# Performance work log

Measured on AMD Instinct MI355X. Metric: run time of the kernel, lower is better.

## Reference

```python
import jax, jax.numpy as jnp
import numpy as np

BLOCK_SIZE = 32
EPS = 1e-6


def setup_inputs() -> dict:
    key = jax.random.key(0)
    k1, k2, k3, k4, k5 = jax.random.split(key, 5)
    B, H, L, D = 2, 16, 4096, 128
    return {
        "query_states": jax.random.normal(k1, (B, H, L, D), dtype=jnp.float32),
        "key_states": jax.random.normal(k2, (B, H, L, D), dtype=jnp.float32),
        "value_states": jax.random.normal(k3, (B, H, L, D), dtype=jnp.float32),
        # learned params; init near torch defaults (ones/zeros) with small noise
        "phi_scale": 1.0 + 0.1 * jax.random.normal(k4, (H, 1, D), dtype=jnp.float32),
        "phi_bias": 0.1 * jax.random.normal(k5, (H, 1, D), dtype=jnp.float32),
    }


def _forward(query_states, key_states, value_states, phi_scale, phi_bias):
    B, H, L, D = query_states.shape
    bs = BLOCK_SIZE
    N = L // bs  # L chosen divisible by block_size (no padding path)

    def feature_map(x):  # x: (B,H,N,bs,D)
        # phi_scale (H,1,D) -> (H,1,1,D) broadcasts over (B,H,N,bs,D)
        y = jax.nn.elu(x * phi_scale[:, None] + phi_bias[:, None]) + 1.0
        return jnp.clip(y, 0.0, 10.0)

    q = query_states.reshape(B, H, N, bs, D)
    k = key_states.reshape(B, H, N, bs, D)
    v = value_states.reshape(B, H, N, bs, D)

    phi_q = feature_map(q)
    phi_k = feature_map(k)

    # move block axis to front for scan: (N,B,H,bs,D)
    pq = jnp.moveaxis(phi_q, 2, 0)
    pk = jnp.moveaxis(phi_k, 2, 0)
    vb = jnp.moveaxis(v, 2, 0)

    S0 = jnp.zeros((B, H, D, D), dtype=jnp.float32)
    Z0 = jnp.zeros((B, H, D), dtype=jnp.float32)

    def step(carry, inp):
        S, Z = carry
        pq_n, pk_n, v_n = inp  # each (B,H,bs,D)
        # block-causal, bidirectional within block: update state BEFORE output
        S = S + jnp.einsum('bhkd,bhke->bhde', pk_n, v_n)
        Z = Z + pk_n.sum(axis=-2)
        num = jnp.einsum('bhqd,bhde->bhqe', pq_n, S)
        den = jnp.maximum(jnp.einsum('bhqd,bhd->bhq', pq_n, Z), EPS)
        return (S, Z), num / den[..., None]

    _, out_blocks = jax.lax.scan(step, (S0, Z0), (pq, pk, vb))  # (N,B,H,bs,D)
    out = jnp.moveaxis(out_blocks, 0, 2).reshape(B, H, L, D)
    return out


def reference(query_states, key_states, value_states, phi_scale, phi_bias):
    return _forward(query_states, key_states, value_states, phi_scale, phi_bias)
```

## Files before the change

kernel.cpp:

```cpp
#include <hip/hip_runtime.h>
#include <stdint.h>

#define BH 32
#define LSEQ 4096
#define DDIM 128
#define BS 32
#define NBLK 128
#define CHUNKS 16
#define BLK_PER_CHUNK 8
#define STATE_SZ (DDIM*DDIM + DDIM)

typedef __attribute__((ext_vector_type(8))) short bf16x8;
typedef __attribute__((ext_vector_type(4))) float f32x4;

__device__ inline uint16_t f2bf(float f) {
    uint32_t x = __builtin_bit_cast(uint32_t, f);
    x += 0x7fffu + ((x >> 16) & 1u);
    return (uint16_t)(x >> 16);
}
__device__ inline float bflo(uint32_t w){ return __builtin_bit_cast(float, w << 16); }
__device__ inline float bfhi(uint32_t w){ return __builtin_bit_cast(float, w & 0xffff0000u); }

__device__ inline float phi_f(float x, float s, float b) {
    float y = fmaf(x, s, b);
    float pos = fminf(y + 1.0f, 10.0f);
    float neg = __expf(y);
    return (y > 0.0f) ? pos : neg;
}

#define SMEM_BYTES 62080

template<bool PHASE2>
__global__ __launch_bounds__(512, 4) void la_phase(
    const float* __restrict__ Q, const float* __restrict__ K,
    const float* __restrict__ V, const float* __restrict__ scale,
    const float* __restrict__ bias, float* __restrict__ states,
    float* __restrict__ out)
{
    extern __shared__ char smem[];
    uint16_t* S_bfT  = (uint16_t*)smem;
    uint16_t* pk_bf  = (uint16_t*)smem;
    uint16_t* v_bf   = (uint16_t*)(smem + 8704);
    uint16_t* pkT    = (uint16_t*)(smem + 34816);
    uint16_t* pq_bf  = pkT;
    uint16_t* vT     = (uint16_t*)(smem + 45056);
    float* Zl        = (float*)(smem + 55296);
    float* Zpart     = Zl + 128;
    float* den_part  = Zpart + 8*128;
    float* inv_den   = den_part + 32*16;

    const int tid  = threadIdx.x;
    const int bid  = blockIdx.x;
    const int bh   = bid >> 4;
    const int ch   = bid & 15;
    const int lane = tid & 63;
    const int wv   = tid >> 6;
    const int i15  = lane & 15;
    const int q4   = lane >> 4;

    const size_t base = (size_t)bh * LSEQ * DDIM;
    const int h = bh & 15;

    const int sr = tid >> 4;
    const int sc = (tid & 15) * 8;

    float sreg[8], breg[8];
    #pragma unroll
    for (int j = 0; j < 8; ++j) {
        sreg[j] = scale[h*DDIM + sc + j];
        breg[j] = bias[h*DDIM + sc + j];
    }

    f32x4 accS[8];
    float* stbase = states + (size_t)(bh*CHUNKS + ch) * STATE_SZ;

    if (PHASE2) {
        #pragma unroll
        for (int mt = 0; mt < 8; ++mt) {
            #pragma unroll
            for (int r = 0; r < 4; ++r) {
                int d = 16*mt + 4*q4 + r;
                accS[mt][r] = stbase[d*DDIM + 16*wv + i15];
            }
        }
        if (tid < 128) Zl[tid] = stbase[DDIM*DDIM + tid];
    } else {
        #pragma unroll
        for (int mt = 0; mt < 8; ++mt) accS[mt] = (f32x4){0.f,0.f,0.f,0.f};
        if (tid < 128) Zl[tid] = 0.f;
    }
    __syncthreads();

    for (int s = 0; s < BLK_PER_CHUNK; ++s) {
        const int blk = ch * BLK_PER_CHUNK + s;
        const size_t rowoff = base + (size_t)(blk*BS + sr) * DDIM + sc;

        {
            const float4 k0 = *(const float4*)(K + rowoff);
            const float4 k1 = *(const float4*)(K + rowoff + 4);
            const float4 v0 = *(const float4*)(V + rowoff);
            const float4 v1 = *(const float4*)(V + rowoff + 4);
            float kp[8] = {k0.x,k0.y,k0.z,k0.w,k1.x,k1.y,k1.z,k1.w};
            float vp[8] = {v0.x,v0.y,v0.z,v0.w,v1.x,v1.y,v1.z,v1.w};
            uint32_t pk[4], pv[4];
            #pragma unroll
            for (int j = 0; j < 4; ++j) {
                uint32_t lo = f2bf(phi_f(kp[2*j],   sreg[2*j],   breg[2*j]));
                uint32_t hi = f2bf(phi_f(kp[2*j+1], sreg[2*j+1], breg[2*j+1]));
                pk[j] = lo | (hi << 16);
                lo = f2bf(vp[2*j]); hi = f2bf(vp[2*j+1]);
                pv[j] = lo | (hi << 16);
            }
            *(uint4*)&pk_bf[sr*136 + sc] = *(uint4*)pk;
            *(uint4*)&v_bf [sr*136 + sc] = *(uint4*)pv;
        }
        __syncthreads();

        {
            const int dp  = tid & 63;
            const int seg = tid >> 6;
            const int r0  = seg * 4;
            uint32_t w0 = *(const uint32_t*)&pk_bf[(r0+0)*136 + 2*dp];
            uint32_t w1 = *(const uint32_t*)&pk_bf[(r0+1)*136 + 2*dp];
            uint32_t w2 = *(const uint32_t*)&pk_bf[(r0+2)*136 + 2*dp];
            uint32_t w3 = *(const uint32_t*)&pk_bf[(r0+3)*136 + 2*dp];
            uint2 lo, hi;
            lo.x = (w0 & 0xffffu) | (w1 << 16);
            lo.y = (w2 & 0xffffu) | (w3 << 16);
            hi.x = (w0 >> 16) | (w1 & 0xffff0000u);
            hi.y = (w2 >> 16) | (w3 & 0xffff0000u);
            *(uint2*)&pkT[(2*dp+0)*40 + r0] = lo;
            *(uint2*)&pkT[(2*dp+1)*40 + r0] = hi;
            Zpart[seg*128 + 2*dp+0] = bflo(w0)+bflo(w1)+bflo(w2)+bflo(w3);
            Zpart[seg*128 + 2*dp+1] = bfhi(w0)+bfhi(w1)+bfhi(w2)+bfhi(w3);
            w0 = *(const uint32_t*)&v_bf[(r0+0)*136 + 2*dp];
            w1 = *(const uint32_t*)&v_bf[(r0+1)*136 + 2*dp];
            w2 = *(const uint32_t*)&v_bf[(r0+2)*136 + 2*dp];
            w3 = *(const uint32_t*)&v_bf[(r0+3)*136 + 2*dp];
            lo.x = (w0 & 0xffffu) | (w1 << 16);
            lo.y = (w2 & 0xffffu) | (w3 << 16);
            hi.x = (w0 >> 16) | (w1 & 0xffff0000u);
            hi.y = (w2 >> 16) | (w3 & 0xffff0000u);
            *(uint2*)&vT[(2*dp+0)*40 + r0] = lo;
            *(uint2*)&vT[(2*dp+1)*40 + r0] = hi;
        }
        __syncthreads();

        if (tid < 128) {
            float z = Zl[tid];
            #pragma unroll
            for (int g = 0; g < 8; ++g) z += Zpart[g*128 + tid];
            Zl[tid] = z;
        }
        {
            bf16x8 bv = *(const bf16x8*)&vT[(16*wv + i15)*40 + 8*q4];
            #pragma unroll
            for (int mt = 0; mt < 8; ++mt) {
                bf16x8 av = *(const bf16x8*)&pkT[(16*mt + i15)*40 + 8*q4];
                accS[mt] = __builtin_amdgcn_mfma_f32_16x16x32_bf16(av, bv, accS[mt], 0, 0, 0);
            }
        }

        if (PHASE2) {
            __syncthreads();

            {
                const float4 a0 = *(const float4*)(Q + rowoff);
                const float4 a1 = *(const float4*)(Q + rowoff + 4);
                float qp[8] = {a0.x,a0.y,a0.z,a0.w,a1.x,a1.y,a1.z,a1.w};
                uint32_t pq[4];
                #pragma unroll
                for (int j = 0; j < 4; ++j) {
                    uint32_t lo = f2bf(phi_f(qp[2*j],   sreg[2*j],   breg[2*j]));
                    uint32_t hi = f2bf(phi_f(qp[2*j+1], sreg[2*j+1], breg[2*j+1]));
                    pq[j] = lo | (hi << 16);
                }
                *(uint4*)&pq_bf[sr*136 + sc] = *(uint4*)pq;
            }
            #pragma unroll
            for (int mt = 0; mt < 8; ++mt) {
                uint2 o;
                o.x = (uint32_t)f2bf(accS[mt][0]) | ((uint32_t)f2bf(accS[mt][1]) << 16);
                o.y = (uint32_t)f2bf(accS[mt][2]) | ((uint32_t)f2bf(accS[mt][3]) << 16);
                *(uint2*)&S_bfT[(16*wv + i15)*136 + 16*mt + 4*q4] = o;
            }
            __syncthreads();

            f32x4 acc2[2];
            acc2[0] = (f32x4){0.f,0.f,0.f,0.f};
            acc2[1] = (f32x4){0.f,0.f,0.f,0.f};
            #pragma unroll
            for (int ks = 0; ks < 4; ++ks) {
                bf16x8 sb = *(const bf16x8*)&S_bfT[(16*wv + i15)*136 + 32*ks + 8*q4];
                #pragma unroll
                for (int qt = 0; qt < 2; ++qt) {
                    bf16x8 qa = *(const bf16x8*)&pq_bf[(16*qt + i15)*136 + 32*ks + 8*q4];
                    acc2[qt] = __builtin_amdgcn_mfma_f32_16x16x32_bf16(qa, sb, acc2[qt], 0, 0, 0);
                }
            }
            {
                const int dq = tid >> 4;
                const int pt = tid & 15;
                float sden = 0.f;
                #pragma unroll
                for (int j = 0; j < 4; ++j) {
                    uint32_t w = *(const uint32_t*)&pq_bf[dq*136 + 8*pt + 2*j];
                    sden += bflo(w) * Zl[8*pt + 2*j] + bfhi(w) * Zl[8*pt + 2*j + 1];
                }
                den_part[dq*16 + pt] = sden;
            }
            __syncthreads();
            if (tid < 32) {
                float sden = 0.f;
                #pragma unroll
                for (int j = 0; j < 16; ++j) sden += den_part[tid*16 + j];
                inv_den[tid] = 1.0f / fmaxf(sden, 1e-6f);
            }
            __syncthreads();

            #pragma unroll
            for (int qt = 0; qt < 2; ++qt) {
                #pragma unroll
                for (int r = 0; r < 4; ++r) {
                    int qrow = 16*qt + 4*q4 + r;
                    float o = acc2[qt][r] * inv_den[qrow];
                    out[base + (size_t)(blk*BS + qrow)*DDIM + 16*wv + i15] = o;
                }
            }
        }
    }

    if (!PHASE2) {
        #pragma unroll
        for (int mt = 0; mt < 8; ++mt) {
            #pragma unroll
            for (int r = 0; r < 4; ++r) {
                int d = 16*mt + 4*q4 + r;
                stbase[d*DDIM + 16*wv + i15] = accS[mt][r];
            }
        }
        if (tid < 128) stbase[DDIM*DDIM + tid] = Zl[tid];
    }
}

__global__ void la_prefix(float* __restrict__ states) {
    const int bh = blockIdx.x >> 4;
    const int sl = blockIdx.x & 15;
    const int slice = STATE_SZ / 16;
    float* p0 = states + (size_t)bh * CHUNKS * STATE_SZ + sl * slice;
    for (int i = threadIdx.x; i < slice; i += 256) {
        float run = 0.f;
        float* p = p0 + i;
        #pragma unroll
        for (int c = 0; c < CHUNKS; ++c) {
            float v = p[(size_t)c * STATE_SZ];
            p[(size_t)c * STATE_SZ] = run;
            run += v;
        }
    }
}

extern "C" void kernel_launch(void* const* d_in, const int* in_sizes, int n_in,
                              void* d_out, int out_size, void* d_ws, size_t ws_size,
                              hipStream_t stream) {
    const float* Q     = (const float*)d_in[0];
    const float* K     = (const float*)d_in[1];
    const float* V     = (const float*)d_in[2];
    const float* scale = (const float*)d_in[3];
    const float* bias  = (const float*)d_in[4];
    float* out    = (float*)d_out;
    float* states = (float*)d_ws;

    hipLaunchKernelGGL((la_phase<false>), dim3(BH*CHUNKS), dim3(512), SMEM_BYTES, stream,
                       Q, K, V, scale, bias, states, out);
    hipLaunchKernelGGL(la_prefix, dim3(BH*16), dim3(256), 0, stream, states);
    hipLaunchKernelGGL((la_phase<true>), dim3(BH*CHUNKS), dim3(512), SMEM_BYTES, stream,
                       Q, K, V, scale, bias, states, out);
}
```

Measured before the change: 271.0 us.

## Prefetch next block into registers, load K/V transposed, and fold denominator into shuffle

Each thread now loads K and V column-wise (one feature, eight rows), so the transposed bf16 tiles are written directly to shared memory. This removes the staging buffer and a transpose pass with its barrier. The next block's K, V and Q are prefetched into registers while the current block computes. The denominator is computed with a wave shuffle reduction instead of a shared-memory partial sum and an extra barrier. Raw barriers that wait only on LDS and MFMA priority hints are added; the cost is more register pressure from the prefetch buffers and uncoalesced-looking column loads.

```diff
diff --git a/kernel.cpp b/kernel.cpp
--- a/kernel.cpp
+++ b/kernel.cpp
@@ -28,7 +28,11 @@
     return (y > 0.0f) ? pos : neg;
 }
 
-#define SMEM_BYTES 62080
+__device__ inline void bar_lgkm() {
+    asm volatile("s_waitcnt lgkmcnt(0)\n\ts_barrier" ::: "memory");
+}
+
+#define SMEM_BYTES 57984
 
 template<bool PHASE2>
 __global__ __launch_bounds__(512, 4) void la_phase(
@@ -38,16 +42,13 @@
     float* __restrict__ out)
 {
     extern __shared__ char smem[];
-    uint16_t* S_bfT  = (uint16_t*)smem;
-    uint16_t* pk_bf  = (uint16_t*)smem;
-    uint16_t* v_bf   = (uint16_t*)(smem + 8704);
-    uint16_t* pkT    = (uint16_t*)(smem + 34816);
-    uint16_t* pq_bf  = pkT;
-    uint16_t* vT     = (uint16_t*)(smem + 45056);
+    uint16_t* pkT    = (uint16_t*)smem;
+    uint16_t* pq_bf  = (uint16_t*)smem;
+    uint16_t* vT     = (uint16_t*)(smem + 10240);
+    uint16_t* S_bfT  = (uint16_t*)(smem + 20480);
     float* Zl        = (float*)(smem + 55296);
     float* Zpart     = Zl + 128;
-    float* den_part  = Zpart + 8*128;
-    float* inv_den   = den_part + 32*16;
+    float* inv_den   = Zpart + 4*128;
 
     const int tid  = threadIdx.x;
     const int bid  = blockIdx.x;
@@ -61,14 +62,20 @@
     const size_t base = (size_t)bh * LSEQ * DDIM;
     const int h = bh & 15;
 
+    const int kd = tid & 127;
+    const int rg = tid >> 7;
     const int sr = tid >> 4;
     const int sc = (tid & 15) * 8;
 
+    const float sk = scale[h*DDIM + kd];
+    const float bk = bias [h*DDIM + kd];
     float sreg[8], breg[8];
-    #pragma unroll
-    for (int j = 0; j < 8; ++j) {
-        sreg[j] = scale[h*DDIM + sc + j];
-        breg[j] = bias[h*DDIM + sc + j];
+    if (PHASE2) {
+        #pragma unroll
+        for (int j = 0; j < 8; ++j) {
+            sreg[j] = scale[h*DDIM + sc + j];
+            breg[j] = bias [h*DDIM + sc + j];
+        }
     }
 
     f32x4 accS[8];
@@ -91,91 +98,90 @@
     }
     __syncthreads();
 
+    float kreg[8], vreg[8], qreg[8];
+    {
+        const size_t coff = base + (size_t)((ch*BLK_PER_CHUNK)*BS + 8*rg)*DDIM + kd;
+        #pragma unroll
+        for (int j = 0; j < 8; ++j) {
+            kreg[j] = K[coff + (size_t)j*DDIM];
+            vreg[j] = V[coff + (size_t)j*DDIM];
+        }
+        if (PHASE2) {
+            const size_t qoff = base + (size_t)((ch*BLK_PER_CHUNK)*BS + sr)*DDIM + sc;
+            const float4 a0 = *(const float4*)(Q + qoff);
+            const float4 a1 = *(const float4*)(Q + qoff + 4);
+            qreg[0]=a0.x; qreg[1]=a0.y; qreg[2]=a0.z; qreg[3]=a0.w;
+            qreg[4]=a1.x; qreg[5]=a1.y; qreg[6]=a1.z; qreg[7]=a1.w;
+        }
+    }
+
     for (int s = 0; s < BLK_PER_CHUNK; ++s) {
         const int blk = ch * BLK_PER_CHUNK + s;
-        const size_t rowoff = base + (size_t)(blk*BS + sr) * DDIM + sc;
 
         {
-            const float4 k0 = *(const float4*)(K + rowoff);
-            const float4 k1 = *(const float4*)(K + rowoff + 4);
-            const float4 v0 = *(const float4*)(V + rowoff);
-            const float4 v1 = *(const float4*)(V + rowoff + 4);
-            float kp[8] = {k0.x,k0.y,k0.z,k0.w,k1.x,k1.y,k1.z,k1.w};
-            float vp[8] = {v0.x,v0.y,v0.z,v0.w,v1.x,v1.y,v1.z,v1.w};
             uint32_t pk[4], pv[4];
+            float zp = 0.f;
             #pragma unroll
             for (int j = 0; j < 4; ++j) {
-                uint32_t lo = f2bf(phi_f(kp[2*j],   sreg[2*j],   breg[2*j]));
-                uint32_t hi = f2bf(phi_f(kp[2*j+1], sreg[2*j+1], breg[2*j+1]));
+                uint32_t lo = f2bf(phi_f(kreg[2*j],   sk, bk));
+                uint32_t hi = f2bf(phi_f(kreg[2*j+1], sk, bk));
                 pk[j] = lo | (hi << 16);
-                lo = f2bf(vp[2*j]); hi = f2bf(vp[2*j+1]);
-                pv[j] = lo | (hi << 16);
-            }
-            *(uint4*)&pk_bf[sr*136 + sc] = *(uint4*)pk;
-            *(uint4*)&v_bf [sr*136 + sc] = *(uint4*)pv;
-        }
-        __syncthreads();
-
-        {
-            const int dp  = tid & 63;
-            const int seg = tid >> 6;
-            const int r0  = seg * 4;
-            uint32_t w0 = *(const uint32_t*)&pk_bf[(r0+0)*136 + 2*dp];
-            uint32_t w1 = *(const uint32_t*)&pk_bf[(r0+1)*136 + 2*dp];
-            uint32_t w2 = *(const uint32_t*)&pk_bf[(r0+2)*136 + 2*dp];
-            uint32_t w3 = *(const uint32_t*)&pk_bf[(r0+3)*136 + 2*dp];
-            uint2 lo, hi;
-            lo.x = (w0 & 0xffffu) | (w1 << 16);
-            lo.y = (w2 & 0xffffu) | (w3 << 16);
-            hi.x = (w0 >> 16) | (w1 & 0xffff0000u);
-            hi.y = (w2 >> 16) | (w3 & 0xffff0000u);
-            *(uint2*)&pkT[(2*dp+0)*40 + r0] = lo;
-            *(uint2*)&pkT[(2*dp+1)*40 + r0] = hi;
-            Zpart[seg*128 + 2*dp+0] = bflo(w0)+bflo(w1)+bflo(w2)+bflo(w3);
-            Zpart[seg*128 + 2*dp+1] = bfhi(w0)+bfhi(w1)+bfhi(w2)+bfhi(w3);
-            w0 = *(const uint32_t*)&v_bf[(r0+0)*136 + 2*dp];
-            w1 = *(const uint32_t*)&v_bf[(r0+1)*136 + 2*dp];
-            w2 = *(const uint32_t*)&v_bf[(r0+2)*136 + 2*dp];
-            w3 = *(const uint32_t*)&v_bf[(r0+3)*136 + 2*dp];
-            lo.x = (w0 & 0xffffu) | (w1 << 16);
-            lo.y = (w2 & 0xffffu) | (w3 << 16);
-            hi.x = (w0 >> 16) | (w1 & 0xffff0000u);
-            hi.y = (w2 >> 16) | (w3 & 0xffff0000u);
-            *(uint2*)&vT[(2*dp+0)*40 + r0] = lo;
-            *(uint2*)&vT[(2*dp+1)*40 + r0] = hi;
-        }
-        __syncthreads();
+                zp += bflo(lo) + bflo(hi);
+                uint32_t vlo = f2bf(vreg[2*j]);
+                uint32_t vhi = f2bf(vreg[2*j+1]);
+                pv[j] = vlo | (vhi << 16);
+            }
+            *(uint4*)&pkT[kd*40 + 8*rg] = *(uint4*)pk;
+            *(uint4*)&vT [kd*40 + 8*rg] = *(uint4*)pv;
+            Zpart[rg*128 + kd] = zp;
+        }
+        if (s + 1 < BLK_PER_CHUNK) {
+            const size_t coff = base + (size_t)((blk+1)*BS + 8*rg)*DDIM + kd;
+            #pragma unroll
+            for (int j = 0; j < 8; ++j) {
+                kreg[j] = K[coff + (size_t)j*DDIM];
+                vreg[j] = V[coff + (size_t)j*DDIM];
+            }
+        }
+        bar_lgkm();
 
         if (tid < 128) {
             float z = Zl[tid];
             #pragma unroll
-            for (int g = 0; g < 8; ++g) z += Zpart[g*128 + tid];
+            for (int g = 0; g < 4; ++g) z += Zpart[g*128 + tid];
             Zl[tid] = z;
         }
         {
             bf16x8 bv = *(const bf16x8*)&vT[(16*wv + i15)*40 + 8*q4];
+            __builtin_amdgcn_s_setprio(1);
             #pragma unroll
             for (int mt = 0; mt < 8; ++mt) {
                 bf16x8 av = *(const bf16x8*)&pkT[(16*mt + i15)*40 + 8*q4];
                 accS[mt] = __builtin_amdgcn_mfma_f32_16x16x32_bf16(av, bv, accS[mt], 0, 0, 0);
             }
+            __builtin_amdgcn_s_setprio(0);
         }
 
         if (PHASE2) {
-            __syncthreads();
+            bar_lgkm();
 
             {
-                const float4 a0 = *(const float4*)(Q + rowoff);
-                const float4 a1 = *(const float4*)(Q + rowoff + 4);
-                float qp[8] = {a0.x,a0.y,a0.z,a0.w,a1.x,a1.y,a1.z,a1.w};
                 uint32_t pq[4];
                 #pragma unroll
                 for (int j = 0; j < 4; ++j) {
-                    uint32_t lo = f2bf(phi_f(qp[2*j],   sreg[2*j],   breg[2*j]));
-                    uint32_t hi = f2bf(phi_f(qp[2*j+1], sreg[2*j+1], breg[2*j+1]));
+                    uint32_t lo = f2bf(phi_f(qreg[2*j],   sreg[2*j],   breg[2*j]));
+                    uint32_t hi = f2bf(phi_f(qreg[2*j+1], sreg[2*j+1], breg[2*j+1]));
                     pq[j] = lo | (hi << 16);
                 }
                 *(uint4*)&pq_bf[sr*136 + sc] = *(uint4*)pq;
+                float sden = 0.f;
+                #pragma unroll
+                for (int j = 0; j < 4; ++j)
+                    sden += bflo(pq[j]) * Zl[sc + 2*j] + bfhi(pq[j]) * Zl[sc + 2*j + 1];
+                #pragma unroll
+                for (int off = 1; off < 16; off <<= 1)
+                    sden += __shfl_xor(sden, off, 64);
+                if ((tid & 15) == 0) inv_den[sr] = 1.0f / fmaxf(sden, 1e-6f);
             }
             #pragma unroll
             for (int mt = 0; mt < 8; ++mt) {
@@ -184,11 +190,19 @@
                 o.y = (uint32_t)f2bf(accS[mt][2]) | ((uint32_t)f2bf(accS[mt][3]) << 16);
                 *(uint2*)&S_bfT[(16*wv + i15)*136 + 16*mt + 4*q4] = o;
             }
-            __syncthreads();
+            if (s + 1 < BLK_PER_CHUNK) {
+                const size_t qoff = base + (size_t)((blk+1)*BS + sr)*DDIM + sc;
+                const float4 a0 = *(const float4*)(Q + qoff);
+                const float4 a1 = *(const float4*)(Q + qoff + 4);
+                qreg[0]=a0.x; qreg[1]=a0.y; qreg[2]=a0.z; qreg[3]=a0.w;
+                qreg[4]=a1.x; qreg[5]=a1.y; qreg[6]=a1.z; qreg[7]=a1.w;
+            }
+            bar_lgkm();
 
             f32x4 acc2[2];
             acc2[0] = (f32x4){0.f,0.f,0.f,0.f};
             acc2[1] = (f32x4){0.f,0.f,0.f,0.f};
+            __builtin_amdgcn_s_setprio(1);
             #pragma unroll
             for (int ks = 0; ks < 4; ++ks) {
                 bf16x8 sb = *(const bf16x8*)&S_bfT[(16*wv + i15)*136 + 32*ks + 8*q4];
@@ -198,25 +212,8 @@
                     acc2[qt] = __builtin_amdgcn_mfma_f32_16x16x32_bf16(qa, sb, acc2[qt], 0, 0, 0);
                 }
             }
-            {
-                const int dq = tid >> 4;
-                const int pt = tid & 15;
-                float sden = 0.f;
-                #pragma unroll
-                for (int j = 0; j < 4; ++j) {
-                    uint32_t w = *(const uint32_t*)&pq_bf[dq*136 + 8*pt + 2*j];
-                    sden += bflo(w) * Zl[8*pt + 2*j] + bfhi(w) * Zl[8*pt + 2*j + 1];
-                }
-                den_part[dq*16 + pt] = sden;
-            }
-            __syncthreads();
-            if (tid < 32) {
-                float sden = 0.f;
-                #pragma unroll
-                for (int j = 0; j < 16; ++j) sden += den_part[tid*16 + j];
-                inv_den[tid] = 1.0f / fmaxf(sden, 1e-6f);
-            }
-            __syncthreads();
+            __builtin_amdgcn_s_setprio(0);
+            bar_lgkm();
 
             #pragma unroll
             for (int qt = 0; qt < 2; ++qt) {
@@ -227,6 +224,8 @@
                     out[base + (size_t)(blk*BS + qrow)*DDIM + 16*wv + i15] = o;
                 }
             }
+        } else {
+            bar_lgkm();
         }
     }
 
```

Result: no change. 275.3 us (+1.6%).
